# Optimization experiments

Hardware: AMD Instinct MI355X
Metric: run time of the kernel (lower is better)

Reference implementation:

```python
import jax, jax.numpy as jnp
import numpy as np

B, T, D, H, L = 8, 150, 30, 5, 3
HD = D // H  # 6
ORIG = (300, 74, 35)


def setup_inputs() -> dict:
    key = jax.random.key(0)
    ks = iter(jax.random.split(key, 40))
    def g(shape, s=0.05):
        return jax.random.normal(next(ks), shape, dtype=jnp.float32) * s
    return {
        "x_l": g((B, T, ORIG[0]), 1.0),
        "x_a": g((B, T, ORIG[1]), 1.0),
        "x_v": g((B, T, ORIG[2]), 1.0),
        "Wl": g((D, ORIG[0])),
        "Wa": g((D, ORIG[1])),
        "Wv": g((D, ORIG[2])),
        "in_w": g((2, L, 3 * D, D)),
        "in_b": jnp.zeros((2, L, 3 * D), jnp.float32),
        "out_w": g((2, L, D, D)),
        "out_b": jnp.zeros((2, L, D), jnp.float32),
        "lin1_w": g((2, L, 4 * D, D)),
        "lin1_b": jnp.zeros((2, L, 4 * D), jnp.float32),
        "lin2_w": g((2, L, D, 4 * D)),
        "lin2_b": jnp.zeros((2, L, D), jnp.float32),
        "n1_g": jnp.ones((2, L, D), jnp.float32),
        "n1_b": jnp.zeros((2, L, D), jnp.float32),
        "n2_g": jnp.ones((2, L, D), jnp.float32),
        "n2_b": jnp.zeros((2, L, D), jnp.float32),
        "p1_w": g((2 * D, 2 * D)),
        "p1_b": jnp.zeros((2 * D,), jnp.float32),
        "p2_w": g((2 * D, 2 * D)),
        "p2_b": jnp.zeros((2 * D,), jnp.float32),
        "ow": g((1, 2 * D)),
        "ob": jnp.zeros((1,), jnp.float32),
    }


def _ln(x, g, b, eps=1e-5):
    m = x.mean(-1, keepdims=True)
    v = jnp.var(x, axis=-1, keepdims=True)  # biased var, matches torch LayerNorm
    return (x - m) * jax.lax.rsqrt(v + eps) * g + b


def _heads(x):  # [Tt, B, D] -> [B*H, Tt, HD]
    Tt = x.shape[0]
    return x.reshape(Tt, B * H, HD).transpose(1, 0, 2)


def _layer(x, xk, xv, p):
    iw, ib, ow, ob, w1, b1, w2, b2, g1, bb1, g2, bb2 = p
    res = x
    xn, kn, vn = _ln(x, g1, bb1), _ln(xk, g1, bb1), _ln(xv, g1, bb1)
    q = (xn @ iw[:D].T + ib[:D]) * (HD ** -0.5)
    k = kn @ iw[D:2 * D].T + ib[D:2 * D]
    v = vn @ iw[2 * D:].T + ib[2 * D:]
    qh, kh, vh = _heads(q), _heads(k), _heads(v)
    # trilinear scores: [B*H, Tq, Tk, Tv]
    aw = jnp.einsum('iat,ibt,ict->iabc', qh, kh, vh)
    fused = aw.mean(-1) + aw.max(-1)          # fuse over value axis -> [B*H, Tq, Tk]
    fused = jax.nn.softmax(fused, axis=-1)
    attn = jnp.einsum('iab,ibt->iat', fused, qh)  # NB: original bmm uses q, not v
    attn = attn.transpose(1, 0, 2).reshape(-1, B, D)
    x = res + (attn @ ow.T + ob)
    res = x
    xn = _ln(x, g2, bb2)
    x = jax.nn.relu(xn @ w1.T + b1) @ w2.T + b2
    return res + x


def reference(x_l, x_a, x_v, Wl, Wa, Wv, in_w, in_b, out_w, out_b,
              lin1_w, lin1_b, lin2_w, lin2_b, n1_g, n1_b, n2_g, n2_b,
              p1_w, p1_b, p2_w, p2_b, ow, ob):
    pl = (x_l @ Wl.T).transpose(1, 0, 2)  # [T, B, D] (conv1d k=1, no bias)
    pa = (x_a @ Wa.T).transpose(1, 0, 2)
    pv = (x_v @ Wv.T).transpose(1, 0, 2)
    hs = []
    for s, (kk, vv) in enumerate(((pa, pv), (pv, pa))):
        h = pl
        for l in range(L):
            p = (in_w[s, l], in_b[s, l], out_w[s, l], out_b[s, l],
                 lin1_w[s, l], lin1_b[s, l], lin2_w[s, l], lin2_b[s, l],
                 n1_g[s, l], n1_b[s, l], n2_g[s, l], n2_b[s, l])
            h = _layer(h, kk, vv, p)
        hs.append(h[-1])  # last timestep [B, D]
    last_hs = jnp.concatenate(hs, axis=1)  # [B, 2D]
    proj = jax.nn.relu(last_hs @ p1_w.T + p1_b) @ p2_w.T + p2_b + last_hs
    out = proj @ ow.T + ob
    return (out, last_hs)
```

## Files before the change

kernel.cpp:

```cpp
#include <hip/hip_runtime.h>
#include <math.h>

#define BB 8
#define TT 150
#define DD 30
#define HH 5
#define HD 6
#define LL 3
#define NI 40
#define ROWF (TT*BB*DD)
#define RSTR 8
#define NR 152

typedef _Float16 half8 __attribute__((ext_vector_type(8)));
typedef float f32x16 __attribute__((ext_vector_type(16)));

__device__ __forceinline__ float wsum(float v) {
    #pragma unroll
    for (int m = 32; m > 0; m >>= 1) v += __shfl_xor(v, m, 64);
    return v;
}

__global__ __launch_bounds__(256) void proj3_kernel(
    const float* __restrict__ x_l, const float* __restrict__ x_a, const float* __restrict__ x_v,
    const float* __restrict__ Wl, const float* __restrict__ Wa, const float* __restrict__ Wv,
    float* __restrict__ pl, float* __restrict__ pa, float* __restrict__ pv) {
    int blk = blockIdx.x;
    int which = blk / 300;
    int w = threadIdx.x >> 6, lane = threadIdx.x & 63;
    int rowu = (blk % 300) * 4 + w;
    int t = rowu / BB, b = rowu % BB;
    const float* x = which == 0 ? x_l : (which == 1 ? x_a : x_v);
    const float* W = which == 0 ? Wl : (which == 1 ? Wa : Wv);
    float* out = which == 0 ? pl : (which == 1 ? pa : pv);
    int Cin = which == 0 ? 300 : (which == 1 ? 74 : 35);
    int cst = Cin | 1;
    __shared__ float WS[30 * 301];
    __shared__ float xr[4][304];
    for (int j = threadIdx.x; j < DD * Cin; j += 256)
        WS[(j / Cin) * cst + (j % Cin)] = W[j];
    const float* xp = x + ((size_t)b * TT + t) * Cin;
    for (int j = lane; j < Cin; j += 64) xr[w][j] = xp[j];
    __syncthreads();
    int d = lane >> 1, jh = lane & 1;
    int h1 = Cin >> 1;
    int j0 = jh ? h1 : 0, j1 = jh ? Cin : h1;
    const float* wr = WS + (size_t)(d < DD ? d : 0) * cst;
    float acc = 0.f;
    for (int j = j0; j < j1; j++) acc += xr[w][j] * wr[j];
    acc += __shfl_xor(acc, 1, 64);
    if (jh == 0 && d < DD) out[t * (BB * DD) + b * DD + d] = acc;
}

__global__ __launch_bounds__(256) void kvq0_kernel(
    const float* __restrict__ pl, const float* __restrict__ pa, const float* __restrict__ pv,
    const float* __restrict__ in_w, const float* __restrict__ in_b,
    const float* __restrict__ n1g, const float* __restrict__ n1b,
    float* __restrict__ k_all, float* __restrict__ v_all, float* __restrict__ q) {
    int blk = blockIdx.x;
    int w = threadIdx.x >> 6, lane = threadIdx.x & 63;
    __shared__ float iwS[1800];
    __shared__ float xn[4][2][30];
    if (blk < 1800) {
        int po = blk / 300;
        int s = po / LL;
        int tb = (blk % 300) * 4 + w;
        int t = tb / BB, b = tb % BB;
        const float* xk = (s == 0) ? pa : pv;
        const float* xv = (s == 0) ? pv : pa;
        const float* iw = in_w + (size_t)po * 2700 + 900;
        const float* ib = in_b + (size_t)po * 90;
        const float* g  = n1g + (size_t)po * 30;
        const float* bb = n1b + (size_t)po * 30;
        for (int j = threadIdx.x; j < 1800; j += 256) iwS[j] = iw[j];
        const float* rows[2] = { xk + (size_t)tb * 30, xv + (size_t)tb * 30 };
        for (int r = 0; r < 2; r++) {
            float xval = (lane < 30) ? rows[r][lane] : 0.f;
            float mean = wsum(xval) * (1.f / 30.f);
            float dv = (lane < 30) ? (xval - mean) : 0.f;
            float var = wsum(dv * dv) * (1.f / 30.f);
            float inv = rsqrtf(var + 1e-5f);
            if (lane < 30) xn[w][r][lane] = dv * inv * g[lane] + bb[lane];
        }
        __syncthreads();
        if (lane < 60) {
            int which = lane / 30, dd = lane % 30;
            const float* wr = iwS + lane * 30;
            const float* xv2 = xn[w][which];
            float acc = 0.f;
            #pragma unroll 6
            for (int j = 0; j < 30; j++) acc += wr[j] * xv2[j];
            acc += ib[30 + lane];
            int i = b * HH + dd / HD, hd = dd % HD;
            float* dst = which ? v_all : k_all;
            dst[((size_t)po * NI + i) * (TT * HD) + t * HD + hd] = acc;
        }
    } else {
        int r2 = blk - 1800;
        int s = r2 / 300;
        int tb = (r2 % 300) * 4 + w;
        int t = tb / BB, b = tb % BB;
        int po = s * LL;
        const float* iw = in_w + (size_t)po * 2700;
        const float* ib = in_b + (size_t)po * 90;
        const float* g  = n1g + (size_t)po * 30;
        const float* bb = n1b + (size_t)po * 30;
        for (int j = threadIdx.x; j < 900; j += 256) iwS[j] = iw[j];
        const float* row = pl + (size_t)tb * 30;
        float xval = (lane < 30) ? row[lane] : 0.f;
        float mean = wsum(xval) * (1.f / 30.f);
        float dv = (lane < 30) ? (xval - mean) : 0.f;
        float var = wsum(dv * dv) * (1.f / 30.f);
        float inv = rsqrtf(var + 1e-5f);
        if (lane < 30) xn[w][0][lane] = dv * inv * g[lane] + bb[lane];
        __syncthreads();
        if (lane < 30) {
            const float* wr = iwS + lane * 30;
            float acc = 0.f;
            #pragma unroll 6
            for (int j = 0; j < 30; j++) acc += wr[j] * xn[w][0][j];
            acc = (acc + ib[lane]) * 0.40824829046386307f;
            int i = b * HH + lane / HD, hd = lane % HD;
            q[((size_t)s * NI + i) * (TT * HD) + t * HD + hd] = acc;
        }
    }
}

__global__ __launch_bounds__(256) void score_kernel(
    const float* __restrict__ q, const float* __restrict__ k_all,
    const float* __restrict__ v_all, int l, float* __restrict__ attn) {
    int blk = blockIdx.x;
    int s = blk / 760;
    int rem = blk % 760;
    int i = rem / 19;
    int g = rem % 19;
    int tid = threadIdx.x;
    int wv = tid >> 6, lane = tid & 63;
    int lo = lane & 31, hf = lane >> 5;
    int po = s * LL + l;

    __shared__ __align__(16) _Float16 qsh[NR * RSTR];
    __shared__ __align__(16) _Float16 ksh[NR * RSTR];
    __shared__ __align__(16) _Float16 vsh[NR * RSTR];

    const float* qg = q + (size_t)(s * NI + i) * (TT * HD);
    const float* kg = k_all + (size_t)(po * NI + i) * (TT * HD);
    const float* vg = v_all + (size_t)(po * NI + i) * (TT * HD);
    half8 z8;
    #pragma unroll
    for (int t = 0; t < 8; t++) z8[t] = (_Float16)0.f;
    for (int r = tid; r < NR; r += 256) {
        half8 qa = z8, ka = z8, va = z8;
        if (r < TT) {
            #pragma unroll
            for (int t = 0; t < 6; t++) {
                qa[t] = (_Float16)qg[r * 6 + t];
                ka[t] = (_Float16)kg[r * 6 + t];
                va[t] = (_Float16)vg[r * 6 + t];
            }
        }
        *(half8*)&qsh[r * RSTR] = qa;
        *(half8*)&ksh[r * RSTR] = ka;
        *(half8*)&vsh[r * RSTR] = va;
    }
    __syncthreads();
    if (wv == 0) {
        float v6[6] = {0.f, 0.f, 0.f, 0.f, 0.f, 0.f};
        for (int c = lane; c < TT; c += 64) {
            #pragma unroll
            for (int t = 0; t < 6; t++) v6[t] += (float)vsh[c * RSTR + t];
        }
        #pragma unroll
        for (int m = 32; m > 0; m >>= 1) {
            #pragma unroll
            for (int t = 0; t < 6; t++) v6[t] += __shfl_xor(v6[t], m, 64);
        }
        if (lane < 6) vsh[TT * RSTR + lane] = (_Float16)(v6[lane] * (1.f / TT));
    }
    __syncthreads();

    f32x16 zacc;
    #pragma unroll
    for (int j = 0; j < 16; j++) zacc[j] = 0.f;

    half8 bfrag[5], vhalf[5];
    #pragma unroll
    for (int nt = 0; nt < 5; nt++) {
        int rr = nt * 32 + lo;
        int rc = rr < 151 ? rr : 151;
        half8 kf = *(const half8*)&ksh[rc * RSTR];
        half8 vf = *(const half8*)&vsh[rc * RSTR];
        bfrag[nt] = hf ? z8 : kf;
        vhalf[nt] = hf ? z8 : vf;
    }

    for (int ap = 0; ap < 2; ap++) {
        int a = g * 8 + wv * 2 + ap;
        if (a >= TT) break;
        half8 qav = *(const half8*)&qsh[a * RSTR];
        half8 afrag[5];
        #pragma unroll
        for (int nt = 0; nt < 5; nt++) afrag[nt] = vhalf[nt] * qav;

        float fsc[5];
        #pragma unroll
        for (int nb = 0; nb < 5; nb++) {
            float rm = -INFINITY;
            #pragma unroll
            for (int ma = 0; ma < 4; ma++) {
                f32x16 acc = __builtin_amdgcn_mfma_f32_32x32x16_f16(afrag[ma], bfrag[nb], zacc, 0, 0, 0);
                float m = fmaxf(acc[0], acc[1]);
                #pragma unroll
                for (int j = 2; j < 16; j += 2) m = fmaxf(fmaxf(m, acc[j]), acc[j + 1]);
                rm = fmaxf(rm, m);
            }
            f32x16 a4 = __builtin_amdgcn_mfma_f32_32x32x16_f16(afrag[4], bfrag[nb], zacc, 0, 0, 0);
            float m4 = fmaxf(a4[0], a4[1]);
            #pragma unroll
            for (int j = 2; j < 10; j += 2) m4 = fmaxf(fmaxf(m4, a4[j]), a4[j + 1]);
            float ext = (hf == 0) ? fmaxf(a4[10], a4[11]) : -INFINITY;
            rm = fmaxf(rm, fmaxf(m4, ext));
            float om = __shfl_xor(a4[10], 32, 64);
            float mn = hf ? a4[10] : om;
            rm = fmaxf(rm, __shfl_xor(rm, 32, 64));
            int bcol = nb * 32 + lo;
            fsc[nb] = (bcol < TT) ? (mn + rm) : -INFINITY;
        }
        float m = fsc[0];
        #pragma unroll
        for (int nb = 1; nb < 5; nb++) m = fmaxf(m, fsc[nb]);
        #pragma unroll
        for (int msk = 16; msk > 0; msk >>= 1) m = fmaxf(m, __shfl_xor(m, msk, 64));
        float e[5], es = 0.f;
        #pragma unroll
        for (int nb = 0; nb < 5; nb++) { e[nb] = __expf(fsc[nb] - m); es += e[nb]; }
        #pragma unroll
        for (int msk = 16; msk > 0; msk >>= 1) es += __shfl_xor(es, msk, 64);
        float acc6[6] = {0.f, 0.f, 0.f, 0.f, 0.f, 0.f};
        #pragma unroll
        for (int nb = 0; nb < 5; nb++) {
            int bcol = nb * 32 + lo;
            int bi = (bcol < TT) ? bcol : 0;
            float wgt = e[nb];
            half8 qrow = *(const half8*)&qsh[bi * RSTR];
            #pragma unroll
            for (int t = 0; t < 6; t++) acc6[t] += wgt * (float)qrow[t];
        }
        #pragma unroll
        for (int msk = 16; msk > 0; msk >>= 1) {
            #pragma unroll
            for (int t = 0; t < 6; t++) acc6[t] += __shfl_xor(acc6[t], msk, 64);
        }
        if (lane == 0) {
            float inv = 1.f / es;
            int bo = i / HH, ho = i % HH;
            float* dst = attn + (size_t)s * ROWF + a * (BB * DD) + bo * DD + ho * HD;
            #pragma unroll
            for (int t = 0; t < 6; t++) dst[t] = acc6[t] * inv;
        }
    }
}

__global__ __launch_bounds__(256) void ffnlnq_kernel(
    const float* __restrict__ attn, const float* __restrict__ pl,
    const float* __restrict__ out_w, const float* __restrict__ out_b,
    const float* __restrict__ l1w, const float* __restrict__ l1b,
    const float* __restrict__ l2w, const float* __restrict__ l2b,
    const float* __restrict__ n2g, const float* __restrict__ n2b,
    const float* __restrict__ in_w, const float* __restrict__ in_b,
    const float* __restrict__ n1g, const float* __restrict__ n1b,
    int l, int has_next,
    float* __restrict__ h, float* __restrict__ q) {
    int blk = blockIdx.x;
    int s = blk / 300;
    int w = threadIdx.x >> 6, lane = threadIdx.x & 63;
    int tb = (blk % 300) * 4 + w;
    int t = tb / BB, b = tb % BB;
    int po = s * LL + l;
    const float* ow = out_w + (size_t)po * 900;
    const float* ob = out_b + (size_t)po * 30;
    const float* w1 = l1w + (size_t)po * 3600;
    const float* b1 = l1b + (size_t)po * 120;
    const float* w2 = l2w + (size_t)po * 3600;
    const float* b2 = l2b + (size_t)po * 30;
    const float* g2 = n2g + (size_t)po * 30;
    const float* bb2 = n2b + (size_t)po * 30;
    __shared__ float owS[900];
    __shared__ float w1T[30 * 128];
    __shared__ float w2S[30 * 121];
    __shared__ float iwqS[900];
    __shared__ float arS[4][30], xnS[4][32], hidS[4][120], xqS[4][30];
    for (int j = threadIdx.x; j < 900; j += 256) owS[j] = ow[j];
    for (int j = threadIdx.x; j < 3600; j += 256) w1T[(j % 30) * 128 + (j / 30)] = w1[j];
    for (int j = threadIdx.x; j < 3600; j += 256) w2S[(j / 120) * 121 + (j % 120)] = w2[j];
    if (has_next) {
        const float* iwq = in_w + (size_t)(po + 1) * 2700;
        for (int j = threadIdx.x; j < 900; j += 256) iwqS[j] = iwq[j];
    }
    __syncthreads();
    float* hrow = h + (size_t)s * ROWF + (size_t)tb * 30;
    const float* res = (l == 0) ? (pl + (size_t)tb * 30) : hrow;
    const float* arow = attn + (size_t)s * ROWF + (size_t)tb * 30;
    if (lane < 30) arS[w][lane] = arow[lane];
    float x1v = 0.f;
    if (lane < 30) {
        const float* wr = owS + lane * 30;
        float acc = 0.f;
        #pragma unroll 6
        for (int j = 0; j < 30; j++) acc += wr[j] * arS[w][j];
        x1v = res[lane] + acc + ob[lane];
    }
    float mean = wsum(x1v) * (1.f / 30.f);
    float dv = (lane < 30) ? (x1v - mean) : 0.f;
    float var = wsum(dv * dv) * (1.f / 30.f);
    float inv = rsqrtf(var + 1e-5f);
    if (lane < 30) xnS[w][lane] = dv * inv * g2[lane] + bb2[lane];
    for (int o = lane; o < 120; o += 64) {
        float acc = 0.f;
        #pragma unroll 6
        for (int j = 0; j < 30; j++) acc += w1T[j * 128 + o] * xnS[w][j];
        hidS[w][o] = fmaxf(acc + b1[o], 0.f);
    }
    float newh = 0.f;
    if (lane < 30) {
        const float* wr = w2S + lane * 121;
        float acc = 0.f;
        #pragma unroll 8
        for (int j = 0; j < 120; j++) acc += wr[j] * hidS[w][j];
        newh = x1v + acc + b2[lane];
        hrow[lane] = newh;
    }
    if (has_next) {
        const float* g1 = n1g + (size_t)(po + 1) * 30;
        const float* bb1 = n1b + (size_t)(po + 1) * 30;
        const float* ibq = in_b + (size_t)(po + 1) * 90;
        float mean2 = wsum(newh) * (1.f / 30.f);
        float dv2 = (lane < 30) ? (newh - mean2) : 0.f;
        float var2 = wsum(dv2 * dv2) * (1.f / 30.f);
        float inv2 = rsqrtf(var2 + 1e-5f);
        if (lane < 30) xqS[w][lane] = dv2 * inv2 * g1[lane] + bb1[lane];
        if (lane < 30) {
            const float* wr = iwqS + lane * 30;
            float acc = 0.f;
            #pragma unroll 6
            for (int j = 0; j < 30; j++) acc += wr[j] * xqS[w][j];
            acc = (acc + ibq[lane]) * 0.40824829046386307f;
            int i = b * HH + lane / HD, hd = lane % HD;
            q[((size_t)s * NI + i) * (TT * HD) + t * HD + hd] = acc;
        }
    }
}

__global__ __launch_bounds__(256) void head_kernel(
    const float* __restrict__ h,
    const float* __restrict__ p1w, const float* __restrict__ p1b,
    const float* __restrict__ p2w, const float* __restrict__ p2b,
    const float* __restrict__ ow, const float* __restrict__ ob,
    float* __restrict__ out) {
    int tid = threadIdx.x;
    __shared__ float lh[480], hid[480], pr[480];
    for (int idx = tid; idx < 480; idx += 256) {
        int b = idx / 60, j = idx % 60;
        int s = j / 30, d = j % 30;
        float vv = h[(size_t)s * ROWF + 149 * (BB * DD) + b * DD + d];
        lh[idx] = vv;
        out[8 + idx] = vv;
    }
    __syncthreads();
    for (int idx = tid; idx < 480; idx += 256) {
        int b = idx / 60, o = idx % 60;
        const float* wr = p1w + o * 60;
        float acc = p1b[o];
        for (int j = 0; j < 60; j++) acc += wr[j] * lh[b * 60 + j];
        hid[idx] = fmaxf(acc, 0.f);
    }
    __syncthreads();
    for (int idx = tid; idx < 480; idx += 256) {
        int b = idx / 60, d = idx % 60;
        const float* wr = p2w + d * 60;
        float acc = p2b[d];
        for (int j = 0; j < 60; j++) acc += wr[j] * hid[b * 60 + j];
        pr[idx] = acc + lh[idx];
    }
    __syncthreads();
    if (tid < 8) {
        float acc = ob[0];
        for (int j = 0; j < 60; j++) acc += pr[tid * 60 + j] * ow[j];
        out[tid] = acc;
    }
}

extern "C" void kernel_launch(void* const* d_in, const int* in_sizes, int n_in,
                              void* d_out, int out_size, void* d_ws, size_t ws_size,
                              hipStream_t stream) {
    const float* x_l   = (const float*)d_in[0];
    const float* x_a   = (const float*)d_in[1];
    const float* x_v   = (const float*)d_in[2];
    const float* Wl    = (const float*)d_in[3];
    const float* Wa    = (const float*)d_in[4];
    const float* Wv    = (const float*)d_in[5];
    const float* in_w  = (const float*)d_in[6];
    const float* in_b  = (const float*)d_in[7];
    const float* out_w = (const float*)d_in[8];
    const float* out_b = (const float*)d_in[9];
    const float* l1w   = (const float*)d_in[10];
    const float* l1b   = (const float*)d_in[11];
    const float* l2w   = (const float*)d_in[12];
    const float* l2b   = (const float*)d_in[13];
    const float* n1g   = (const float*)d_in[14];
    const float* n1b   = (const float*)d_in[15];
    const float* n2g   = (const float*)d_in[16];
    const float* n2b   = (const float*)d_in[17];
    const float* p1w   = (const float*)d_in[18];
    const float* p1b   = (const float*)d_in[19];
    const float* p2w   = (const float*)d_in[20];
    const float* p2b   = (const float*)d_in[21];
    const float* oww   = (const float*)d_in[22];
    const float* obb   = (const float*)d_in[23];

    float* ws = (float*)d_ws;
    float* pl    = ws;
    float* pa    = ws + 36000;
    float* pv    = ws + 72000;
    float* h     = ws + 108000;
    float* q     = ws + 180000;
    float* k_all = ws + 252000;
    float* v_all = ws + 468000;
    float* at    = ws + 684000;

    proj3_kernel<<<900, 256, 0, stream>>>(x_l, x_a, x_v, Wl, Wa, Wv, pl, pa, pv);
    kvq0_kernel<<<2400, 256, 0, stream>>>(pl, pa, pv, in_w, in_b, n1g, n1b,
                                          k_all, v_all, q);
    for (int l = 0; l < LL; l++) {
        score_kernel<<<1520, 256, 0, stream>>>(q, k_all, v_all, l, at);
        ffnlnq_kernel<<<600, 256, 0, stream>>>(at, pl, out_w, out_b, l1w, l1b, l2w, l2b,
                                               n2g, n2b, in_w, in_b, n1g, n1b,
                                               l, (l < LL - 1) ? 1 : 0, h, q);
    }
    head_kernel<<<1, 256, 0, stream>>>(h, p1w, p1b, p2w, p2b, oww, obb, (float*)d_out);
}
```

Before: 247.7 us.

## Fuse all stages into one cooperative persistent kernel with grid syncs

Merges the projection, KVQ, per-layer score and FFN kernels and the head into a single cooperative kernel. Each stage runs as a grid-stride loop over the old block indices, separated by grid.sync(), and all stages share one union of shared memory. The aim is to remove the launch overhead and inter-kernel gaps of eight separate launches. The score loader also now reads q/k/v as float2. In exchange, grid size is capped by occupancy, which the large shared union may lower, and grid-wide barriers add their own cost.

```diff
diff --git a/kernel.cpp b/kernel.cpp
--- a/kernel.cpp
+++ b/kernel.cpp
@@ -1,5 +1,8 @@
 #include <hip/hip_runtime.h>
+#include <hip/hip_cooperative_groups.h>
 #include <math.h>
+
+namespace cg = cooperative_groups;
 
 #define BB 8
 #define TT 150
@@ -15,427 +18,441 @@
 typedef _Float16 half8 __attribute__((ext_vector_type(8)));
 typedef float f32x16 __attribute__((ext_vector_type(16)));
 
+union SMem {
+    struct { float WS[30 * 301]; float xr[4][304]; } proj;
+    struct { float iwS[1800]; float xn[4][2][30]; } kvq;
+    struct { __align__(16) _Float16 qsh[NR * RSTR];
+             __align__(16) _Float16 ksh[NR * RSTR];
+             __align__(16) _Float16 vsh[NR * RSTR]; } sc;
+    struct { float owS[900]; float w1T[30 * 128]; float w2S[30 * 121]; float iwqS[900];
+             float arS[4][30]; float xnS[4][32]; float hidS[4][120]; float xqS[4][30]; } ffn;
+    struct { float lh[480]; float hid[480]; float pr[480]; } head;
+};
+
+struct MegaParams {
+    const float *x_l, *x_a, *x_v, *Wl, *Wa, *Wv;
+    const float *in_w, *in_b, *out_w, *out_b;
+    const float *l1w, *l1b, *l2w, *l2b;
+    const float *n1g, *n1b, *n2g, *n2b;
+    const float *p1w, *p1b, *p2w, *p2b, *oww, *obb;
+    float *pl, *pa, *pv, *h, *q, *k_all, *v_all, *at, *out;
+};
+
 __device__ __forceinline__ float wsum(float v) {
     #pragma unroll
     for (int m = 32; m > 0; m >>= 1) v += __shfl_xor(v, m, 64);
     return v;
 }
 
-__global__ __launch_bounds__(256) void proj3_kernel(
-    const float* __restrict__ x_l, const float* __restrict__ x_a, const float* __restrict__ x_v,
-    const float* __restrict__ Wl, const float* __restrict__ Wa, const float* __restrict__ Wv,
-    float* __restrict__ pl, float* __restrict__ pa, float* __restrict__ pv) {
-    int blk = blockIdx.x;
-    int which = blk / 300;
-    int w = threadIdx.x >> 6, lane = threadIdx.x & 63;
-    int rowu = (blk % 300) * 4 + w;
-    int t = rowu / BB, b = rowu % BB;
-    const float* x = which == 0 ? x_l : (which == 1 ? x_a : x_v);
-    const float* W = which == 0 ? Wl : (which == 1 ? Wa : Wv);
-    float* out = which == 0 ? pl : (which == 1 ? pa : pv);
-    int Cin = which == 0 ? 300 : (which == 1 ? 74 : 35);
-    int cst = Cin | 1;
-    __shared__ float WS[30 * 301];
-    __shared__ float xr[4][304];
-    for (int j = threadIdx.x; j < DD * Cin; j += 256)
-        WS[(j / Cin) * cst + (j % Cin)] = W[j];
-    const float* xp = x + ((size_t)b * TT + t) * Cin;
-    for (int j = lane; j < Cin; j += 64) xr[w][j] = xp[j];
-    __syncthreads();
-    int d = lane >> 1, jh = lane & 1;
-    int h1 = Cin >> 1;
-    int j0 = jh ? h1 : 0, j1 = jh ? Cin : h1;
-    const float* wr = WS + (size_t)(d < DD ? d : 0) * cst;
-    float acc = 0.f;
-    for (int j = j0; j < j1; j++) acc += xr[w][j] * wr[j];
-    acc += __shfl_xor(acc, 1, 64);
-    if (jh == 0 && d < DD) out[t * (BB * DD) + b * DD + d] = acc;
-}
-
-__global__ __launch_bounds__(256) void kvq0_kernel(
-    const float* __restrict__ pl, const float* __restrict__ pa, const float* __restrict__ pv,
-    const float* __restrict__ in_w, const float* __restrict__ in_b,
-    const float* __restrict__ n1g, const float* __restrict__ n1b,
-    float* __restrict__ k_all, float* __restrict__ v_all, float* __restrict__ q) {
-    int blk = blockIdx.x;
-    int w = threadIdx.x >> 6, lane = threadIdx.x & 63;
-    __shared__ float iwS[1800];
-    __shared__ float xn[4][2][30];
-    if (blk < 1800) {
-        int po = blk / 300;
-        int s = po / LL;
-        int tb = (blk % 300) * 4 + w;
-        int t = tb / BB, b = tb % BB;
-        const float* xk = (s == 0) ? pa : pv;
-        const float* xv = (s == 0) ? pv : pa;
-        const float* iw = in_w + (size_t)po * 2700 + 900;
-        const float* ib = in_b + (size_t)po * 90;
-        const float* g  = n1g + (size_t)po * 30;
-        const float* bb = n1b + (size_t)po * 30;
-        for (int j = threadIdx.x; j < 1800; j += 256) iwS[j] = iw[j];
-        const float* rows[2] = { xk + (size_t)tb * 30, xv + (size_t)tb * 30 };
-        for (int r = 0; r < 2; r++) {
-            float xval = (lane < 30) ? rows[r][lane] : 0.f;
+__global__ __launch_bounds__(256) void mega(MegaParams p) {
+    __shared__ SMem sm;
+    cg::grid_group grid = cg::this_grid();
+    const int tid = threadIdx.x;
+    const int w = tid >> 6, lane = tid & 63;
+
+    for (int u = blockIdx.x; u < 900; u += gridDim.x) {
+        int which = u / 300;
+        int rowu = (u % 300) * 4 + w;
+        int t = rowu / BB, b = rowu % BB;
+        const float* x = which == 0 ? p.x_l : (which == 1 ? p.x_a : p.x_v);
+        const float* W = which == 0 ? p.Wl : (which == 1 ? p.Wa : p.Wv);
+        float* out = which == 0 ? p.pl : (which == 1 ? p.pa : p.pv);
+        int Cin = which == 0 ? 300 : (which == 1 ? 74 : 35);
+        int cst = Cin | 1;
+        float* WS = sm.proj.WS;
+        for (int j = tid; j < DD * Cin; j += 256)
+            WS[(j / Cin) * cst + (j % Cin)] = W[j];
+        const float* xp = x + ((size_t)b * TT + t) * Cin;
+        for (int j = lane; j < Cin; j += 64) sm.proj.xr[w][j] = xp[j];
+        __syncthreads();
+        int d = lane >> 1, jh = lane & 1;
+        int h1 = Cin >> 1;
+        int j0 = jh ? h1 : 0, j1 = jh ? Cin : h1;
+        const float* wr = WS + (size_t)(d < DD ? d : 0) * cst;
+        float acc = 0.f;
+        for (int j = j0; j < j1; j++) acc += sm.proj.xr[w][j] * wr[j];
+        acc += __shfl_xor(acc, 1, 64);
+        if (jh == 0 && d < DD) out[t * (BB * DD) + b * DD + d] = acc;
+        __syncthreads();
+    }
+    grid.sync();
+
+    for (int u = blockIdx.x; u < 2400; u += gridDim.x) {
+        float* iwS = sm.kvq.iwS;
+        if (u < 1800) {
+            int po = u / 300;
+            int s = po / LL;
+            int tb = (u % 300) * 4 + w;
+            int t = tb / BB, b = tb % BB;
+            const float* xk = (s == 0) ? p.pa : p.pv;
+            const float* xv = (s == 0) ? p.pv : p.pa;
+            const float* iw = p.in_w + (size_t)po * 2700 + 900;
+            const float* ib = p.in_b + (size_t)po * 90;
+            const float* g  = p.n1g + (size_t)po * 30;
+            const float* bb = p.n1b + (size_t)po * 30;
+            for (int j = tid; j < 1800; j += 256) iwS[j] = iw[j];
+            const float* rows[2] = { xk + (size_t)tb * 30, xv + (size_t)tb * 30 };
+            for (int r = 0; r < 2; r++) {
+                float xval = (lane < 30) ? rows[r][lane] : 0.f;
+                float mean = wsum(xval) * (1.f / 30.f);
+                float dv = (lane < 30) ? (xval - mean) : 0.f;
+                float var = wsum(dv * dv) * (1.f / 30.f);
+                float inv = rsqrtf(var + 1e-5f);
+                if (lane < 30) sm.kvq.xn[w][r][lane] = dv * inv * g[lane] + bb[lane];
+            }
+            __syncthreads();
+            if (lane < 60) {
+                int which = lane / 30, dd = lane % 30;
+                const float* wr = iwS + lane * 30;
+                const float* xv2 = sm.kvq.xn[w][which];
+                float acc = 0.f;
+                #pragma unroll 6
+                for (int j = 0; j < 30; j++) acc += wr[j] * xv2[j];
+                acc += ib[30 + lane];
+                int i = b * HH + dd / HD, hd = dd % HD;
+                float* dst = which ? p.v_all : p.k_all;
+                dst[((size_t)po * NI + i) * (TT * HD) + t * HD + hd] = acc;
+            }
+        } else {
+            int r2 = u - 1800;
+            int s = r2 / 300;
+            int tb = (r2 % 300) * 4 + w;
+            int t = tb / BB, b = tb % BB;
+            int po = s * LL;
+            const float* iw = p.in_w + (size_t)po * 2700;
+            const float* ib = p.in_b + (size_t)po * 90;
+            const float* g  = p.n1g + (size_t)po * 30;
+            const float* bb = p.n1b + (size_t)po * 30;
+            for (int j = tid; j < 900; j += 256) iwS[j] = iw[j];
+            const float* row = p.pl + (size_t)tb * 30;
+            float xval = (lane < 30) ? row[lane] : 0.f;
             float mean = wsum(xval) * (1.f / 30.f);
             float dv = (lane < 30) ? (xval - mean) : 0.f;
             float var = wsum(dv * dv) * (1.f / 30.f);
             float inv = rsqrtf(var + 1e-5f);
-            if (lane < 30) xn[w][r][lane] = dv * inv * g[lane] + bb[lane];
-        }
-        __syncthreads();
-        if (lane < 60) {
-            int which = lane / 30, dd = lane % 30;
-            const float* wr = iwS + lane * 30;
-            const float* xv2 = xn[w][which];
-            float acc = 0.f;
-            #pragma unroll 6
-            for (int j = 0; j < 30; j++) acc += wr[j] * xv2[j];
-            acc += ib[30 + lane];
-            int i = b * HH + dd / HD, hd = dd % HD;
-            float* dst = which ? v_all : k_all;
-            dst[((size_t)po * NI + i) * (TT * HD) + t * HD + hd] = acc;
-        }
-    } else {
-        int r2 = blk - 1800;
-        int s = r2 / 300;
-        int tb = (r2 % 300) * 4 + w;
-        int t = tb / BB, b = tb % BB;
-        int po = s * LL;
-        const float* iw = in_w + (size_t)po * 2700;
-        const float* ib = in_b + (size_t)po * 90;
-        const float* g  = n1g + (size_t)po * 30;
-        const float* bb = n1b + (size_t)po * 30;
-        for (int j = threadIdx.x; j < 900; j += 256) iwS[j] = iw[j];
-        const float* row = pl + (size_t)tb * 30;
-        float xval = (lane < 30) ? row[lane] : 0.f;
-        float mean = wsum(xval) * (1.f / 30.f);
-        float dv = (lane < 30) ? (xval - mean) : 0.f;
-        float var = wsum(dv * dv) * (1.f / 30.f);
-        float inv = rsqrtf(var + 1e-5f);
-        if (lane < 30) xn[w][0][lane] = dv * inv * g[lane] + bb[lane];
-        __syncthreads();
-        if (lane < 30) {
-            const float* wr = iwS + lane * 30;
-            float acc = 0.f;
-            #pragma unroll 6
-            for (int j = 0; j < 30; j++) acc += wr[j] * xn[w][0][j];
-            acc = (acc + ib[lane]) * 0.40824829046386307f;
-            int i = b * HH + lane / HD, hd = lane % HD;
-            q[((size_t)s * NI + i) * (TT * HD) + t * HD + hd] = acc;
-        }
+            if (lane < 30) sm.kvq.xn[w][0][lane] = dv * inv * g[lane] + bb[lane];
+            __syncthreads();
+            if (lane < 30) {
+                const float* wr = iwS + lane * 30;
+                float acc = 0.f;
+                #pragma unroll 6
+                for (int j = 0; j < 30; j++) acc += wr[j] * sm.kvq.xn[w][0][j];
+                acc = (acc + ib[lane]) * 0.40824829046386307f;
+                int i = b * HH + lane / HD, hd = lane % HD;
+                p.q[((size_t)s * NI + i) * (TT * HD) + t * HD + hd] = acc;
+            }
+        }
+        __syncthreads();
     }
-}
-
-__global__ __launch_bounds__(256) void score_kernel(
-    const float* __restrict__ q, const float* __restrict__ k_all,
-    const float* __restrict__ v_all, int l, float* __restrict__ attn) {
-    int blk = blockIdx.x;
-    int s = blk / 760;
-    int rem = blk % 760;
-    int i = rem / 19;
-    int g = rem % 19;
-    int tid = threadIdx.x;
-    int wv = tid >> 6, lane = tid & 63;
-    int lo = lane & 31, hf = lane >> 5;
-    int po = s * LL + l;
-
-    __shared__ __align__(16) _Float16 qsh[NR * RSTR];
-    __shared__ __align__(16) _Float16 ksh[NR * RSTR];
-    __shared__ __align__(16) _Float16 vsh[NR * RSTR];
-
-    const float* qg = q + (size_t)(s * NI + i) * (TT * HD);
-    const float* kg = k_all + (size_t)(po * NI + i) * (TT * HD);
-    const float* vg = v_all + (size_t)(po * NI + i) * (TT * HD);
-    half8 z8;
-    #pragma unroll
-    for (int t = 0; t < 8; t++) z8[t] = (_Float16)0.f;
-    for (int r = tid; r < NR; r += 256) {
-        half8 qa = z8, ka = z8, va = z8;
-        if (r < TT) {
+
+    for (int l = 0; l < LL; l++) {
+        grid.sync();
+        for (int u = blockIdx.x; u < 1520; u += gridDim.x) {
+            int s = u / 760;
+            int rem = u % 760;
+            int i = rem / 19;
+            int g = rem % 19;
+            int lo = lane & 31, hf = lane >> 5;
+            int po = s * LL + l;
+            _Float16* qsh = sm.sc.qsh;
+            _Float16* ksh = sm.sc.ksh;
+            _Float16* vsh = sm.sc.vsh;
+
+            const float* qg = p.q + (size_t)(s * NI + i) * (TT * HD);
+            const float* kg = p.k_all + (size_t)(po * NI + i) * (TT * HD);
+            const float* vg = p.v_all + (size_t)(po * NI + i) * (TT * HD);
+            half8 z8;
             #pragma unroll
-            for (int t = 0; t < 6; t++) {
-                qa[t] = (_Float16)qg[r * 6 + t];
-                ka[t] = (_Float16)kg[r * 6 + t];
-                va[t] = (_Float16)vg[r * 6 + t];
-            }
-        }
-        *(half8*)&qsh[r * RSTR] = qa;
-        *(half8*)&ksh[r * RSTR] = ka;
-        *(half8*)&vsh[r * RSTR] = va;
+            for (int t = 0; t < 8; t++) z8[t] = (_Float16)0.f;
+            for (int r = tid; r < NR; r += 256) {
+                half8 qa = z8, ka = z8, va = z8;
+                if (r < TT) {
+                    const float2* q2 = (const float2*)qg + r * 3;
+                    const float2* k2 = (const float2*)kg + r * 3;
+                    const float2* v2 = (const float2*)vg + r * 3;
+                    float2 a0 = q2[0], a1 = q2[1], a2 = q2[2];
+                    qa[0] = (_Float16)a0.x; qa[1] = (_Float16)a0.y;
+                    qa[2] = (_Float16)a1.x; qa[3] = (_Float16)a1.y;
+                    qa[4] = (_Float16)a2.x; qa[5] = (_Float16)a2.y;
+                    float2 b0 = k2[0], b1 = k2[1], b2 = k2[2];
+                    ka[0] = (_Float16)b0.x; ka[1] = (_Float16)b0.y;
+                    ka[2] = (_Float16)b1.x; ka[3] = (_Float16)b1.y;
+                    ka[4] = (_Float16)b2.x; ka[5] = (_Float16)b2.y;
+                    float2 c0 = v2[0], c1 = v2[1], c2 = v2[2];
+                    va[0] = (_Float16)c0.x; va[1] = (_Float16)c0.y;
+                    va[2] = (_Float16)c1.x; va[3] = (_Float16)c1.y;
+                    va[4] = (_Float16)c2.x; va[5] = (_Float16)c2.y;
+                }
+                *(half8*)&qsh[r * RSTR] = qa;
+                *(half8*)&ksh[r * RSTR] = ka;
+                *(half8*)&vsh[r * RSTR] = va;
+            }
+            __syncthreads();
+            if (w == 0) {
+                float v6[6] = {0.f, 0.f, 0.f, 0.f, 0.f, 0.f};
+                for (int c = lane; c < TT; c += 64) {
+                    #pragma unroll
+                    for (int t = 0; t < 6; t++) v6[t] += (float)vsh[c * RSTR + t];
+                }
+                #pragma unroll
+                for (int m = 32; m > 0; m >>= 1) {
+                    #pragma unroll
+                    for (int t = 0; t < 6; t++) v6[t] += __shfl_xor(v6[t], m, 64);
+                }
+                if (lane < 6) vsh[TT * RSTR + lane] = (_Float16)(v6[lane] * (1.f / TT));
+            }
+            __syncthreads();
+
+            f32x16 zacc;
+            #pragma unroll
+            for (int j = 0; j < 16; j++) zacc[j] = 0.f;
+
+            half8 bfrag[5], vhalf[5];
+            #pragma unroll
+            for (int nt = 0; nt < 5; nt++) {
+                int rr = nt * 32 + lo;
+                int rc = rr < 151 ? rr : 151;
+                half8 kf = *(const half8*)&ksh[rc * RSTR];
+                half8 vf = *(const half8*)&vsh[rc * RSTR];
+                bfrag[nt] = hf ? z8 : kf;
+                vhalf[nt] = hf ? z8 : vf;
+            }
+
+            for (int ap = 0; ap < 2; ap++) {
+                int a = g * 8 + w * 2 + ap;
+                if (a >= TT) break;
+                half8 qav = *(const half8*)&qsh[a * RSTR];
+                half8 afrag[5];
+                #pragma unroll
+                for (int nt = 0; nt < 5; nt++) afrag[nt] = vhalf[nt] * qav;
+
+                float fsc[5];
+                #pragma unroll
+                for (int nb = 0; nb < 5; nb++) {
+                    float rm = -INFINITY;
+                    #pragma unroll
+                    for (int ma = 0; ma < 4; ma++) {
+                        f32x16 acc = __builtin_amdgcn_mfma_f32_32x32x16_f16(afrag[ma], bfrag[nb], zacc, 0, 0, 0);
+                        float m = fmaxf(acc[0], acc[1]);
+                        #pragma unroll
+                        for (int j = 2; j < 16; j += 2) m = fmaxf(fmaxf(m, acc[j]), acc[j + 1]);
+                        rm = fmaxf(rm, m);
+                    }
+                    f32x16 a4 = __builtin_amdgcn_mfma_f32_32x32x16_f16(afrag[4], bfrag[nb], zacc, 0, 0, 0);
+                    float m4 = fmaxf(a4[0], a4[1]);
+                    #pragma unroll
+                    for (int j = 2; j < 10; j += 2) m4 = fmaxf(fmaxf(m4, a4[j]), a4[j + 1]);
+                    float ext = (hf == 0) ? fmaxf(a4[10], a4[11]) : -INFINITY;
+                    rm = fmaxf(rm, fmaxf(m4, ext));
+                    float om = __shfl_xor(a4[10], 32, 64);
+                    float mn = hf ? a4[10] : om;
+                    rm = fmaxf(rm, __shfl_xor(rm, 32, 64));
+                    int bcol = nb * 32 + lo;
+                    fsc[nb] = (bcol < TT) ? (mn + rm) : -INFINITY;
+                }
+                float m = fsc[0];
+                #pragma unroll
+                for (int nb = 1; nb < 5; nb++) m = fmaxf(m, fsc[nb]);
+                #pragma unroll
+                for (int msk = 16; msk > 0; msk >>= 1) m = fmaxf(m, __shfl_xor(m, msk, 64));
+                float e[5], es = 0.f;
+                #pragma unroll
+                for (int nb = 0; nb < 5; nb++) { e[nb] = __expf(fsc[nb] - m); es += e[nb]; }
+                #pragma unroll
+                for (int msk = 16; msk > 0; msk >>= 1) es += __shfl_xor(es, msk, 64);
+                float acc6[6] = {0.f, 0.f, 0.f, 0.f, 0.f, 0.f};
+                #pragma unroll
+                for (int nb = 0; nb < 5; nb++) {
+                    int bcol = nb * 32 + lo;
+                    int bi = (bcol < TT) ? bcol : 0;
+                    float wgt = e[nb];
+                    half8 qrow = *(const half8*)&qsh[bi * RSTR];
+                    #pragma unroll
+                    for (int t = 0; t < 6; t++) acc6[t] += wgt * (float)qrow[t];
+                }
+                #pragma unroll
+                for (int msk = 16; msk > 0; msk >>= 1) {
+                    #pragma unroll
+                    for (int t = 0; t < 6; t++) acc6[t] += __shfl_xor(acc6[t], msk, 64);
+                }
+                if (lane == 0) {
+                    float inv = 1.f / es;
+                    int bo = i / HH, ho = i % HH;
+                    float* dst = p.at + (size_t)s * ROWF + a * (BB * DD) + bo * DD + ho * HD;
+                    #pragma unroll
+                    for (int t = 0; t < 6; t++) dst[t] = acc6[t] * inv;
+                }
+            }
+            __syncthreads();
+        }
+        grid.sync();
+        int has_next = (l < LL - 1) ? 1 : 0;
+        for (int u = blockIdx.x; u < 600; u += gridDim.x) {
+            int s = u / 300;
+            int tb = (u % 300) * 4 + w;
+            int t = tb / BB, b = tb % BB;
+            int po = s * LL + l;
+            const float* ow = p.out_w + (size_t)po * 900;
+            const float* ob = p.out_b + (size_t)po * 30;
+            const float* w1 = p.l1w + (size_t)po * 3600;
+            const float* b1 = p.l1b + (size_t)po * 120;
+            const float* w2 = p.l2w + (size_t)po * 3600;
+            const float* b2 = p.l2b + (size_t)po * 30;
+            const float* g2 = p.n2g + (size_t)po * 30;
+            const float* bb2 = p.n2b + (size_t)po * 30;
+            for (int j = tid; j < 900; j += 256) sm.ffn.owS[j] = ow[j];
+            for (int j = tid; j < 3600; j += 256) sm.ffn.w1T[(j % 30) * 128 + (j / 30)] = w1[j];
+            for (int j = tid; j < 3600; j += 256) sm.ffn.w2S[(j / 120) * 121 + (j % 120)] = w2[j];
+            if (has_next) {
+                const float* iwq = p.in_w + (size_t)(po + 1) * 2700;
+                for (int j = tid; j < 900; j += 256) sm.ffn.iwqS[j] = iwq[j];
+            }
+            __syncthreads();
+            float* hrow = p.h + (size_t)s * ROWF + (size_t)tb * 30;
+            const float* res = (l == 0) ? (p.pl + (size_t)tb * 30) : hrow;
+            const float* arow = p.at + (size_t)s * ROWF + (size_t)tb * 30;
+            if (lane < 30) sm.ffn.arS[w][lane] = arow[lane];
+            float x1v = 0.f;
+            if (lane < 30) {
+                const float* wr = sm.ffn.owS + lane * 30;
+                float acc = 0.f;
+                #pragma unroll 6
+                for (int j = 0; j < 30; j++) acc += wr[j] * sm.ffn.arS[w][j];
+                x1v = res[lane] + acc + ob[lane];
+            }
+            float mean = wsum(x1v) * (1.f / 30.f);
+            float dv = (lane < 30) ? (x1v - mean) : 0.f;
+            float var = wsum(dv * dv) * (1.f / 30.f);
+            float inv = rsqrtf(var + 1e-5f);
+            if (lane < 30) sm.ffn.xnS[w][lane] = dv * inv * g2[lane] + bb2[lane];
+            for (int o = lane; o < 120; o += 64) {
+                float acc = 0.f;
+                #pragma unroll 6
+                for (int j = 0; j < 30; j++) acc += sm.ffn.w1T[j * 128 + o] * sm.ffn.xnS[w][j];
+                sm.ffn.hidS[w][o] = fmaxf(acc + b1[o], 0.f);
+            }
+            float newh = 0.f;
+            if (lane < 30) {
+                const float* wr = sm.ffn.w2S + lane * 121;
+                float acc = 0.f;
+                #pragma unroll 8
+                for (int j = 0; j < 120; j++) acc += wr[j] * sm.ffn.hidS[w][j];
+                newh = x1v + acc + b2[lane];
+                hrow[lane] = newh;
+            }
+            if (has_next) {
+                const float* g1 = p.n1g + (size_t)(po + 1) * 30;
+                const float* bb1 = p.n1b + (size_t)(po + 1) * 30;
+                const float* ibq = p.in_b + (size_t)(po + 1) * 90;
+                float mean2 = wsum(newh) * (1.f / 30.f);
+                float dv2 = (lane < 30) ? (newh - mean2) : 0.f;
+                float var2 = wsum(dv2 * dv2) * (1.f / 30.f);
+                float inv2 = rsqrtf(var2 + 1e-5f);
+                if (lane < 30) sm.ffn.xqS[w][lane] = dv2 * inv2 * g1[lane] + bb1[lane];
+                if (lane < 30) {
+                    const float* wr = sm.ffn.iwqS + lane * 30;
+                    float acc = 0.f;
+                    #pragma unroll 6
+                    for (int j = 0; j < 30; j++) acc += wr[j] * sm.ffn.xqS[w][j];
+                    acc = (acc + ibq[lane]) * 0.40824829046386307f;
+                    int i = b * HH + lane / HD, hd = lane % HD;
+                    p.q[((size_t)s * NI + i) * (TT * HD) + t * HD + hd] = acc;
+                }
+            }
+            __syncthreads();
+        }
     }
-    __syncthreads();
-    if (wv == 0) {
-        float v6[6] = {0.f, 0.f, 0.f, 0.f, 0.f, 0.f};
-        for (int c = lane; c < TT; c += 64) {
-            #pragma unroll
-            for (int t = 0; t < 6; t++) v6[t] += (float)vsh[c * RSTR + t];
-        }
-        #pragma unroll
-        for (int m = 32; m > 0; m >>= 1) {
-            #pragma unroll
-            for (int t = 0; t < 6; t++) v6[t] += __shfl_xor(v6[t], m, 64);
-        }
-        if (lane < 6) vsh[TT * RSTR + lane] = (_Float16)(v6[lane] * (1.f / TT));
-    }
-    __syncthreads();
-
-    f32x16 zacc;
-    #pragma unroll
-    for (int j = 0; j < 16; j++) zacc[j] = 0.f;
-
-    half8 bfrag[5], vhalf[5];
-    #pragma unroll
-    for (int nt = 0; nt < 5; nt++) {
-        int rr = nt * 32 + lo;
-        int rc = rr < 151 ? rr : 151;
-        half8 kf = *(const half8*)&ksh[rc * RSTR];
-        half8 vf = *(const half8*)&vsh[rc * RSTR];
-        bfrag[nt] = hf ? z8 : kf;
-        vhalf[nt] = hf ? z8 : vf;
-    }
-
-    for (int ap = 0; ap < 2; ap++) {
-        int a = g * 8 + wv * 2 + ap;
-        if (a >= TT) break;
-        half8 qav = *(const half8*)&qsh[a * RSTR];
-        half8 afrag[5];
-        #pragma unroll
-        for (int nt = 0; nt < 5; nt++) afrag[nt] = vhalf[nt] * qav;
-
-        float fsc[5];
-        #pragma unroll
-        for (int nb = 0; nb < 5; nb++) {
-            float rm = -INFINITY;
-            #pragma unroll
-            for (int ma = 0; ma < 4; ma++) {
-                f32x16 acc = __builtin_amdgcn_mfma_f32_32x32x16_f16(afrag[ma], bfrag[nb], zacc, 0, 0, 0);
-                float m = fmaxf(acc[0], acc[1]);
-                #pragma unroll
-                for (int j = 2; j < 16; j += 2) m = fmaxf(fmaxf(m, acc[j]), acc[j + 1]);
-                rm = fmaxf(rm, m);
-            }
-            f32x16 a4 = __builtin_amdgcn_mfma_f32_32x32x16_f16(afrag[4], bfrag[nb], zacc, 0, 0, 0);
-            float m4 = fmaxf(a4[0], a4[1]);
-            #pragma unroll
-            for (int j = 2; j < 10; j += 2) m4 = fmaxf(fmaxf(m4, a4[j]), a4[j + 1]);
-            float ext = (hf == 0) ? fmaxf(a4[10], a4[11]) : -INFINITY;
-            rm = fmaxf(rm, fmaxf(m4, ext));
-            float om = __shfl_xor(a4[10], 32, 64);
-            float mn = hf ? a4[10] : om;
-            rm = fmaxf(rm, __shfl_xor(rm, 32, 64));
-            int bcol = nb * 32 + lo;
-            fsc[nb] = (bcol < TT) ? (mn + rm) : -INFINITY;
-        }
-        float m = fsc[0];
-        #pragma unroll
-        for (int nb = 1; nb < 5; nb++) m = fmaxf(m, fsc[nb]);
-        #pragma unroll
-        for (int msk = 16; msk > 0; msk >>= 1) m = fmaxf(m, __shfl_xor(m, msk, 64));
-        float e[5], es = 0.f;
-        #pragma unroll
-        for (int nb = 0; nb < 5; nb++) { e[nb] = __expf(fsc[nb] - m); es += e[nb]; }
-        #pragma unroll
-        for (int msk = 16; msk > 0; msk >>= 1) es += __shfl_xor(es, msk, 64);
-        float acc6[6] = {0.f, 0.f, 0.f, 0.f, 0.f, 0.f};
-        #pragma unroll
-        for (int nb = 0; nb < 5; nb++) {
-            int bcol = nb * 32 + lo;
-            int bi = (bcol < TT) ? bcol : 0;
-            float wgt = e[nb];
-            half8 qrow = *(const half8*)&qsh[bi * RSTR];
-            #pragma unroll
-            for (int t = 0; t < 6; t++) acc6[t] += wgt * (float)qrow[t];
-        }
-        #pragma unroll
-        for (int msk = 16; msk > 0; msk >>= 1) {
-            #pragma unroll
-            for (int t = 0; t < 6; t++) acc6[t] += __shfl_xor(acc6[t], msk, 64);
-        }
-        if (lane == 0) {
-            float inv = 1.f / es;
-            int bo = i / HH, ho = i % HH;
-            float* dst = attn + (size_t)s * ROWF + a * (BB * DD) + bo * DD + ho * HD;
-            #pragma unroll
-            for (int t = 0; t < 6; t++) dst[t] = acc6[t] * inv;
-        }
-    }
-}
-
-__global__ __launch_bounds__(256) void ffnlnq_kernel(
-    const float* __restrict__ attn, const float* __restrict__ pl,
-    const float* __restrict__ out_w, const float* __restrict__ out_b,
-    const float* __restrict__ l1w, const float* __restrict__ l1b,
-    const float* __restrict__ l2w, const float* __restrict__ l2b,
-    const float* __restrict__ n2g, const float* __restrict__ n2b,
-    const float* __restrict__ in_w, const float* __restrict__ in_b,
-    const float* __restrict__ n1g, const float* __restrict__ n1b,
-    int l, int has_next,
-    float* __restrict__ h, float* __restrict__ q) {
-    int blk = blockIdx.x;
-    int s = blk / 300;
-    int w = threadIdx.x >> 6, lane = threadIdx.x & 63;
-    int tb = (blk % 300) * 4 + w;
-    int t = tb / BB, b = tb % BB;
-    int po = s * LL + l;
-    const float* ow = out_w + (size_t)po * 900;
-    const float* ob = out_b + (size_t)po * 30;
-    const float* w1 = l1w + (size_t)po * 3600;
-    const float* b1 = l1b + (size_t)po * 120;
-    const float* w2 = l2w + (size_t)po * 3600;
-    const float* b2 = l2b + (size_t)po * 30;
-    const float* g2 = n2g + (size_t)po * 30;
-    const float* bb2 = n2b + (size_t)po * 30;
-    __shared__ float owS[900];
-    __shared__ float w1T[30 * 128];
-    __shared__ float w2S[30 * 121];
-    __shared__ float iwqS[900];
-    __shared__ float arS[4][30], xnS[4][32], hidS[4][120], xqS[4][30];
-    for (int j = threadIdx.x; j < 900; j += 256) owS[j] = ow[j];
-    for (int j = threadIdx.x; j < 3600; j += 256) w1T[(j % 30) * 128 + (j / 30)] = w1[j];
-    for (int j = threadIdx.x; j < 3600; j += 256) w2S[(j / 120) * 121 + (j % 120)] = w2[j];
-    if (has_next) {
-        const float* iwq = in_w + (size_t)(po + 1) * 2700;
-        for (int j = threadIdx.x; j < 900; j += 256) iwqS[j] = iwq[j];
-    }
-    __syncthreads();
-    float* hrow = h + (size_t)s * ROWF + (size_t)tb * 30;
-    const float* res = (l == 0) ? (pl + (size_t)tb * 30) : hrow;
-    const float* arow = attn + (size_t)s * ROWF + (size_t)tb * 30;
-    if (lane < 30) arS[w][lane] = arow[lane];
-    float x1v = 0.f;
-    if (lane < 30) {
-        const float* wr = owS + lane * 30;
-        float acc = 0.f;
-        #pragma unroll 6
-        for (int j = 0; j < 30; j++) acc += wr[j] * arS[w][j];
-        x1v = res[lane] + acc + ob[lane];
-    }
-    float mean = wsum(x1v) * (1.f / 30.f);
-    float dv = (lane < 30) ? (x1v - mean) : 0.f;
-    float var = wsum(dv * dv) * (1.f / 30.f);
-    float inv = rsqrtf(var + 1e-5f);
-    if (lane < 30) xnS[w][lane] = dv * inv * g2[lane] + bb2[lane];
-    for (int o = lane; o < 120; o += 64) {
-        float acc = 0.f;
-        #pragma unroll 6
-        for (int j = 0; j < 30; j++) acc += w1T[j * 128 + o] * xnS[w][j];
-        hidS[w][o] = fmaxf(acc + b1[o], 0.f);
-    }
-    float newh = 0.f;
-    if (lane < 30) {
-        const float* wr = w2S + lane * 121;
-        float acc = 0.f;
-        #pragma unroll 8
-        for (int j = 0; j < 120; j++) acc += wr[j] * hidS[w][j];
-        newh = x1v + acc + b2[lane];
-        hrow[lane] = newh;
-    }
-    if (has_next) {
-        const float* g1 = n1g + (size_t)(po + 1) * 30;
-        const float* bb1 = n1b + (size_t)(po + 1) * 30;
-        const float* ibq = in_b + (size_t)(po + 1) * 90;
-        float mean2 = wsum(newh) * (1.f / 30.f);
-        float dv2 = (lane < 30) ? (newh - mean2) : 0.f;
-        float var2 = wsum(dv2 * dv2) * (1.f / 30.f);
-        float inv2 = rsqrtf(var2 + 1e-5f);
-        if (lane < 30) xqS[w][lane] = dv2 * inv2 * g1[lane] + bb1[lane];
-        if (lane < 30) {
-            const float* wr = iwqS + lane * 30;
-            float acc = 0.f;
-            #pragma unroll 6
-            for (int j = 0; j < 30; j++) acc += wr[j] * xqS[w][j];
-            acc = (acc + ibq[lane]) * 0.40824829046386307f;
-            int i = b * HH + lane / HD, hd = lane % HD;
-            q[((size_t)s * NI + i) * (TT * HD) + t * HD + hd] = acc;
-        }
-    }
-}
-
-__global__ __launch_bounds__(256) void head_kernel(
-    const float* __restrict__ h,
-    const float* __restrict__ p1w, const float* __restrict__ p1b,
-    const float* __restrict__ p2w, const float* __restrict__ p2b,
-    const float* __restrict__ ow, const float* __restrict__ ob,
-    float* __restrict__ out) {
-    int tid = threadIdx.x;
-    __shared__ float lh[480], hid[480], pr[480];
-    for (int idx = tid; idx < 480; idx += 256) {
-        int b = idx / 60, j = idx % 60;
-        int s = j / 30, d = j % 30;
-        float vv = h[(size_t)s * ROWF + 149 * (BB * DD) + b * DD + d];
-        lh[idx] = vv;
-        out[8 + idx] = vv;
-    }
-    __syncthreads();
-    for (int idx = tid; idx < 480; idx += 256) {
-        int b = idx / 60, o = idx % 60;
-        const float* wr = p1w + o * 60;
-        float acc = p1b[o];
-        for (int j = 0; j < 60; j++) acc += wr[j] * lh[b * 60 + j];
-        hid[idx] = fmaxf(acc, 0.f);
-    }
-    __syncthreads();
-    for (int idx = tid; idx < 480; idx += 256) {
-        int b = idx / 60, d = idx % 60;
-        const float* wr = p2w + d * 60;
-        float acc = p2b[d];
-        for (int j = 0; j < 60; j++) acc += wr[j] * hid[b * 60 + j];
-        pr[idx] = acc + lh[idx];
-    }
-    __syncthreads();
-    if (tid < 8) {
-        float acc = ob[0];
-        for (int j = 0; j < 60; j++) acc += pr[tid * 60 + j] * ow[j];
-        out[tid] = acc;
+    grid.sync();
+
+    if (blockIdx.x == 0) {
+        for (int idx = tid; idx < 480; idx += 256) {
+            int b = idx / 60, j = idx % 60;
+            int s = j / 30, d = j % 30;
+            float vv = p.h[(size_t)s * ROWF + 149 * (BB * DD) + b * DD + d];
+            sm.head.lh[idx] = vv;
+            p.out[8 + idx] = vv;
+        }
+        __syncthreads();
+        for (int idx = tid; idx < 480; idx += 256) {
+            int b = idx / 60, o = idx % 60;
+            const float* wr = p.p1w + o * 60;
+            float acc = p.p1b[o];
+            for (int j = 0; j < 60; j++) acc += wr[j] * sm.head.lh[b * 60 + j];
+            sm.head.hid[idx] = fmaxf(acc, 0.f);
+        }
+        __syncthreads();
+        for (int idx = tid; idx < 480; idx += 256) {
+            int b = idx / 60, d = idx % 60;
+            const float* wr = p.p2w + d * 60;
+            float acc = p.p2b[d];
+            for (int j = 0; j < 60; j++) acc += wr[j] * sm.head.hid[b * 60 + j];
+            sm.head.pr[idx] = acc + sm.head.lh[idx];
+        }
+        __syncthreads();
+        if (tid < 8) {
+            float acc = p.obb[0];
+            for (int j = 0; j < 60; j++) acc += sm.head.pr[tid * 60 + j] * p.oww[j];
+            p.out[tid] = acc;
+        }
     }
 }
 
 extern "C" void kernel_launch(void* const* d_in, const int* in_sizes, int n_in,
                               void* d_out, int out_size, void* d_ws, size_t ws_size,
                               hipStream_t stream) {
-    const float* x_l   = (const float*)d_in[0];
-    const float* x_a   = (const float*)d_in[1];
-    const float* x_v   = (const float*)d_in[2];
-    const float* Wl    = (const float*)d_in[3];
-    const float* Wa    = (const float*)d_in[4];
-    const float* Wv    = (const float*)d_in[5];
-    const float* in_w  = (const float*)d_in[6];
-    const float* in_b  = (const float*)d_in[7];
-    const float* out_w = (const float*)d_in[8];
-    const float* out_b = (const float*)d_in[9];
-    const float* l1w   = (const float*)d_in[10];
-    const float* l1b   = (const float*)d_in[11];
-    const float* l2w   = (const float*)d_in[12];
-    const float* l2b   = (const float*)d_in[13];
-    const float* n1g   = (const float*)d_in[14];
-    const float* n1b   = (const float*)d_in[15];
-    const float* n2g   = (const float*)d_in[16];
-    const float* n2b   = (const float*)d_in[17];
-    const float* p1w   = (const float*)d_in[18];
-    const float* p1b   = (const float*)d_in[19];
-    const float* p2w   = (const float*)d_in[20];
-    const float* p2b   = (const float*)d_in[21];
-    const float* oww   = (const float*)d_in[22];
-    const float* obb   = (const float*)d_in[23];
-
     float* ws = (float*)d_ws;
-    float* pl    = ws;
-    float* pa    = ws + 36000;
-    float* pv    = ws + 72000;
-    float* h     = ws + 108000;
-    float* q     = ws + 180000;
-    float* k_all = ws + 252000;
-    float* v_all = ws + 468000;
-    float* at    = ws + 684000;
-
-    proj3_kernel<<<900, 256, 0, stream>>>(x_l, x_a, x_v, Wl, Wa, Wv, pl, pa, pv);
-    kvq0_kernel<<<2400, 256, 0, stream>>>(pl, pa, pv, in_w, in_b, n1g, n1b,
-                                          k_all, v_all, q);
-    for (int l = 0; l < LL; l++) {
-        score_kernel<<<1520, 256, 0, stream>>>(q, k_all, v_all, l, at);
-        ffnlnq_kernel<<<600, 256, 0, stream>>>(at, pl, out_w, out_b, l1w, l1b, l2w, l2b,
-                                               n2g, n2b, in_w, in_b, n1g, n1b,
-                                               l, (l < LL - 1) ? 1 : 0, h, q);
+
+    MegaParams p;
+    p.x_l   = (const float*)d_in[0];
+    p.x_a   = (const float*)d_in[1];
+    p.x_v   = (const float*)d_in[2];
+    p.Wl    = (const float*)d_in[3];
+    p.Wa    = (const float*)d_in[4];
+    p.Wv    = (const float*)d_in[5];
+    p.in_w  = (const float*)d_in[6];
+    p.in_b  = (const float*)d_in[7];
+    p.out_w = (const float*)d_in[8];
+    p.out_b = (const float*)d_in[9];
+    p.l1w   = (const float*)d_in[10];
+    p.l1b   = (const float*)d_in[11];
+    p.l2w   = (const float*)d_in[12];
+    p.l2b   = (const float*)d_in[13];
+    p.n1g   = (const float*)d_in[14];
+    p.n1b   = (const float*)d_in[15];
+    p.n2g   = (const float*)d_in[16];
+    p.n2b   = (const float*)d_in[17];
+    p.p1w   = (const float*)d_in[18];
+    p.p1b   = (const float*)d_in[19];
+    p.p2w   = (const float*)d_in[20];
+    p.p2b   = (const float*)d_in[21];
+    p.oww   = (const float*)d_in[22];
+    p.obb   = (const float*)d_in[23];
+
+    p.pl    = ws;
+    p.pa    = ws + 36000;
+    p.pv    = ws + 72000;
+    p.h     = ws + 108000;
+    p.q     = ws + 180000;
+    p.k_all = ws + 252000;
+    p.v_all = ws + 468000;
+    p.at    = ws + 684000;
+    p.out   = (float*)d_out;
+
+    static int gridN = 0;
+    if (gridN == 0) {
+        int dev = 0;
+        hipGetDevice(&dev);
+        int nb = 0, ncu = 0;
+        hipOccupancyMaxActiveBlocksPerMultiprocessor(&nb, mega, 256, 0);
+        hipDeviceGetAttribute(&ncu, hipDeviceAttributeMultiprocessorCount, dev);
+        if (nb < 1) nb = 1;
+        if (ncu < 1) ncu = 256;
+        long g = (long)nb * (long)ncu;
+        if (g > 1520) g = 1520;
+        if (g < 1) g = 1;
+        gridN = (int)g;
     }
-    head_kernel<<<1, 256, 0, stream>>>(h, p1w, p1b, p2w, p2b, oww, obb, (float*)d_out);
+
+    void* args[] = { (void*)&p };
+    hipLaunchCooperativeKernel((void*)mega, dim3(gridN), dim3(256), args, 0, stream);
 }
```

Measured after the change: 622.1 us. 151% more time.
